# Performance work log

Measured on AMD Instinct MI355X. Metric: run time of the kernel, lower is better.

## Reference

```python
import jax, jax.numpy as jnp
import numpy as np

EPS = 1e-5
NUM_HEADS = 8

def _bn(x, w, b, m, v):
    # inference-mode BatchNorm2d over channel dim of (B,C,H,W)
    inv = w / jnp.sqrt(v + EPS)
    return x * inv[None, :, None, None] + (b - m * inv)[None, :, None, None]

def _conv1x1(x, W, b):
    # 1x1 conv == per-pixel matmul: W is (out_ch, in_ch)
    return jnp.einsum('bchw,ec->behw', x, W) + b[None, :, None, None]

def _forward(x, bn1_w, bn1_b, bn1_m, bn1_v, Wq, bq, Wk, bk, Wv, bv, gamma, temperature,
             conv_w, conv_b, cbn_w, cbn_b, cbn_m, cbn_v, rs_w, rs_b, rbn_w, rbn_b, rbn_m, rbn_v):
    B, C, Wd, Hd = x.shape
    S = Wd * Hd
    E = Wq.shape[0]
    hd = E // NUM_HEADS
    xa = jax.nn.relu(_bn(x, bn1_w, bn1_b, bn1_m, bn1_v))
    def proj(Wm, bm):
        return _conv1x1(xa, Wm, bm).reshape(B, NUM_HEADS, hd, S).transpose(0, 1, 3, 2)  # (B,h,S,d)
    q = proj(Wq, bq)
    k = proj(Wk, bk)
    v = proj(Wv, bv)
    scores = jnp.einsum('bhsd,bhtd->bhst', q, k) / temperature  # (B,h,S,S)
    scores = scores - jnp.max(scores, axis=-1, keepdims=True)   # redundant amax-subtract as in source
    attn = jax.nn.softmax(scores, axis=-1)
    out = jnp.einsum('bhst,bhtd->bhsd', attn, v)
    out = out.transpose(0, 1, 3, 2).reshape(B, E, Wd, Hd)
    conv_path = jax.nn.relu(_bn(_conv1x1(x, conv_w, conv_b), cbn_w, cbn_b, cbn_m, cbn_v))
    fused = gamma[0] * out + conv_path
    return jax.nn.gelu(_bn(_conv1x1(fused, rs_w, rs_b), rbn_w, rbn_b, rbn_m, rbn_v), approximate=False)

def setup_inputs() -> dict:
    key = jax.random.key(0)
    ks = jax.random.split(key, 18)
    C, E = 256, 512
    n = lambda k, s, sc=0.02: jax.random.normal(k, s, jnp.float32) * sc
    return {
        'x': jax.random.normal(ks[0], (1, C, 64, 64), jnp.float32),
        'bn1_w': 1.0 + n(ks[1], (C,), 0.1), 'bn1_b': n(ks[2], (C,), 0.1),
        'bn1_m': n(ks[3], (C,), 0.05), 'bn1_v': 0.5 + jax.random.uniform(ks[4], (C,), jnp.float32),
        'Wq': n(ks[5], (E, C)), 'bq': jnp.zeros((E,), jnp.float32),
        'Wk': n(ks[6], (E, C)), 'bk': jnp.zeros((E,), jnp.float32),
        'Wv': n(ks[7], (E, C)), 'bv': jnp.zeros((E,), jnp.float32),
        'gamma': jnp.full((1,), 0.5, jnp.float32),
        'temperature': jnp.asarray(0.85, jnp.float32),
        'conv_w': n(ks[8], (E, C)), 'conv_b': jnp.zeros((E,), jnp.float32),
        'cbn_w': 1.0 + n(ks[9], (E,), 0.1), 'cbn_b': n(ks[10], (E,), 0.1),
        'cbn_m': n(ks[11], (E,), 0.05), 'cbn_v': 0.5 + jax.random.uniform(ks[12], (E,), jnp.float32),
        'rs_w': n(ks[13], (C, E)), 'rs_b': jnp.zeros((C,), jnp.float32),
        'rbn_w': 1.0 + n(ks[14], (C,), 0.1), 'rbn_b': n(ks[15], (C,), 0.1),
        'rbn_m': n(ks[16], (C,), 0.05), 'rbn_v': 0.5 + jax.random.uniform(ks[17], (C,), jnp.float32),
    }

def reference(x, bn1_w, bn1_b, bn1_m, bn1_v, Wq, bq, Wk, bk, Wv, bv, gamma, temperature,
              conv_w, conv_b, cbn_w, cbn_b, cbn_m, cbn_v, rs_w, rs_b, rbn_w, rbn_b, rbn_m, rbn_v):
    return _forward(x, bn1_w, bn1_b, bn1_m, bn1_v, Wq, bq, Wk, bk, Wv, bv, gamma, temperature,
                    conv_w, conv_b, cbn_w, cbn_b, cbn_m, cbn_v, rs_w, rs_b, rbn_w, rbn_b, rbn_m, rbn_v)
```

## Files before the change

### kernel.cpp

```cpp
#include <hip/hip_runtime.h>

#define S_DIM 4096
#define C_IN  256
#define E_DIM 512
#define HD    64
#define EPSV  1e-5f

typedef __attribute__((ext_vector_type(8))) short s8v;
typedef __attribute__((ext_vector_type(4))) short s4v;
typedef __attribute__((ext_vector_type(4))) float f4v;
typedef __attribute__((ext_vector_type(16))) float f16v;

__device__ __forceinline__ float bf2f(unsigned short h){
  union{unsigned u; float f;} v; v.u = ((unsigned)h)<<16; return v.f;
}
__device__ __forceinline__ unsigned short f2bf(float f){
  union{float f; unsigned u;} v; v.f = f;
  unsigned r = v.u + 0x7fffu + ((v.u>>16)&1u);
  return (unsigned short)(r>>16);
}
__device__ __forceinline__ unsigned cvtpk_bf16(float lo, float hi_){
  unsigned r;
  asm("v_cvt_pk_bf16_f32 %0, %1, %2" : "=v"(r) : "v"(lo), "v"(hi_));
  return r;
}
__device__ __forceinline__ s8v lds_rd8(const unsigned short* b, int row, int ck){
  return *(const s8v*)&b[(row<<6) + (((ck)^(row&7))<<3)];
}
__device__ __forceinline__ s4v lds_rd4(const unsigned short* b, int row, int eoff){
  int ck = eoff>>3, sub = eoff&7;
  return *(const s4v*)&b[(row<<6) + ((ck^(row&7))<<3) + sub];
}
__device__ __forceinline__ void lds_wr8(unsigned short* b, int row, int ck, s8v v){
  *(s8v*)&b[(row<<6) + (((ck)^(row&7))<<3)] = v;
}

__global__ __launch_bounds__(256) void k_wcvt(const float* __restrict__ w0,
    const float* __restrict__ w1, const float* __restrict__ w2,
    const float* __restrict__ w3, const float* __restrict__ w4,
    unsigned short* __restrict__ dst){
  int i = blockIdx.x*256 + threadIdx.x;
  int z = blockIdx.y;
  const float* s = (z==0)?w0:(z==1)?w1:(z==2)?w2:(z==3)?w3:w4;
  dst[z*(E_DIM*C_IN) + i] = f2bf(s[i]);
}

__global__ __launch_bounds__(256) void k_prep(const float* __restrict__ x,
    const float* __restrict__ bw, const float* __restrict__ bb,
    const float* __restrict__ bm, const float* __restrict__ bvar,
    unsigned short* __restrict__ XaT, unsigned short* __restrict__ XrT){
  __shared__ float tile[32][33];
  int tid = threadIdx.x;
  int tx = tid & 31, ty = tid >> 5;
  int s0 = blockIdx.x*32, c0 = blockIdx.y*32;
  #pragma unroll
  for(int p=0;p<4;p++){
    int c = c0 + ty + p*8;
    tile[ty+p*8][tx] = x[c*S_DIM + s0 + tx];
  }
  __syncthreads();
  int cc = c0 + tx;
  float inv  = bw[cc] * rsqrtf(bvar[cc] + EPSV);
  float beta = bb[cc] - bm[cc]*inv;
  #pragma unroll
  for(int p=0;p<4;p++){
    int s = s0 + ty + p*8;
    float v = tile[tx][ty+p*8];
    float a = v*inv + beta; a = a>0.f?a:0.f;
    XaT[s*C_IN + cc] = f2bf(a);
    XrT[s*C_IN + cc] = f2bf(v);
  }
}

__global__ __launch_bounds__(256) void k_proj(
    const unsigned short* __restrict__ XaT, const unsigned short* __restrict__ XrT,
    const unsigned short* __restrict__ Wb,
    const float* __restrict__ bq, const float* __restrict__ bk,
    const float* __restrict__ bvb, const float* __restrict__ bc,
    const float* __restrict__ cw, const float* __restrict__ cbb,
    const float* __restrict__ cm, const float* __restrict__ cvv,
    unsigned short* __restrict__ QT, unsigned short* __restrict__ KT,
    unsigned short* __restrict__ Vx, unsigned short* __restrict__ CT){
  int z = blockIdx.z;
  const unsigned short* Xin = (z==3) ? XrT : XaT;
  const unsigned short* W   = Wb + z*(E_DIM*C_IN);
  const float* bias = (z==0)?bq:(z==1)?bk:(z==2)?bvb:bc;

  __shared__ unsigned short Als[128*64];
  __shared__ unsigned short Bls[64*64];
  int tid = threadIdx.x;
  int w = tid>>6, l = tid&63, g = l>>4, c16 = l&15;
  int wr = w>>1, wc = w&1;
  int s0 = blockIdx.x*128, e0 = blockIdx.y*64;

  f4v acc[4][2];
  #pragma unroll
  for(int m=0;m<4;m++)
    #pragma unroll
    for(int n=0;n<2;n++) acc[m][n] = (f4v){0.f,0.f,0.f,0.f};

  for(int kk=0;kk<4;kk++){
    __syncthreads();
    #pragma unroll
    for(int p=0;p<4;p++){
      int ck = p*256 + tid, row = ck>>3, ch = ck&7;
      s8v v = *(const s8v*)&Xin[(s0+row)*C_IN + kk*64 + ch*8];
      lds_wr8(Als, row, ch, v);
    }
    #pragma unroll
    for(int p=0;p<2;p++){
      int ck = p*256 + tid, row = ck>>3, ch = ck&7;
      s8v v = *(const s8v*)&W[(e0+row)*C_IN + kk*64 + ch*8];
      lds_wr8(Bls, row, ch, v);
    }
    __syncthreads();
    #pragma unroll
    for(int kb=0;kb<2;kb++){
      s8v bfr[2];
      #pragma unroll
      for(int n=0;n<2;n++) bfr[n] = lds_rd8(Bls, wc*32 + n*16 + c16, g + kb*4);
      #pragma unroll
      for(int m=0;m<4;m++){
        s8v af = lds_rd8(Als, wr*64 + m*16 + c16, g + kb*4);
        #pragma unroll
        for(int n=0;n<2;n++)
          acc[m][n] = __builtin_amdgcn_mfma_f32_16x16x32_bf16(af, bfr[n], acc[m][n], 0,0,0);
      }
    }
  }
  #pragma unroll
  for(int n=0;n<2;n++){
    int e = e0 + wc*32 + n*16 + c16;
    float bsv = bias[e];
    float cinv = 0.f, cbeta = 0.f;
    if(z==3){ cinv = cw[e]*rsqrtf(cvv[e]+EPSV); cbeta = cbb[e] - cm[e]*cinv; }
    #pragma unroll
    for(int m=0;m<4;m++){
      int sb = s0 + wr*64 + m*16 + g*4;
      if(z==2){
        s4v pk;
        #pragma unroll
        for(int i=0;i<4;i++) pk[i] = (short)f2bf(acc[m][n][i] + bsv);
        *(s4v*)&Vx[e*S_DIM + sb] = pk;
      } else {
        unsigned short* dst = (z==0)?QT:(z==1)?KT:CT;
        #pragma unroll
        for(int i=0;i<4;i++){
          float vv = acc[m][n][i] + bsv;
          if(z==3){ vv = vv*cinv + cbeta; vv = vv>0.f?vv:0.f; }
          dst[(sb+i)*E_DIM + e] = f2bf(vv);
        }
      }
    }
  }
}

__global__ __launch_bounds__(256) void k_attn(
    const unsigned short* __restrict__ QT, const unsigned short* __restrict__ KT,
    const unsigned short* __restrict__ Vx, const unsigned short* __restrict__ CT,
    const float* __restrict__ gamma, const float* __restrict__ temp,
    unsigned short* __restrict__ fusedT){
  __shared__ unsigned short SM[4*4096];
  int tid = threadIdx.x;
  int w = tid>>6, l = tid&63, l31 = l&31, hi = l>>5;
  int qh = w&1, kh = w>>1;
  int h = blockIdx.y;
  int qb = blockIdx.x*64;
  int q = qb + qh*32 + l31;
  float scl = 1.0f / temp[0];

  const unsigned short* Kb = SM + kh*4096;
  const unsigned short* Vb = SM + 8192 + kh*4096;

  s8v qf[4];
  #pragma unroll
  for(int ks=0;ks<4;ks++){
    s8v r = *(const s8v*)&QT[q*E_DIM + h*HD + ks*16 + hi*8];
    #pragma unroll
    for(int j=0;j<8;j++) qf[ks][j] = (short)f2bf(bf2f((unsigned short)r[j])*scl);
  }

  f16v oacc0, oacc1;
  #pragma unroll
  for(int r=0;r<16;r++){ oacc0[r]=0.f; oacc1[r]=0.f; }
  float lrun = 0.f;

  for(int t=0;t<32;t++){
    __syncthreads();
    #pragma unroll
    for(int p=0;p<8;p++){
      int flat = p*256 + tid;
      int tile = flat>>9, cid = flat&511, row = cid>>3, ch = cid&7;
      int khp = tile&1, isV = tile>>1;
      int sK = ((khp<<5) + t)<<6;
      s8v v;
      if(!isV) v = *(const s8v*)&KT[(sK+row)*E_DIM + h*HD + ch*8];
      else     v = *(const s8v*)&Vx[(h*HD+row)*S_DIM + sK + ch*8];
      lds_wr8(SM + tile*4096, row, ch, v);
    }
    __syncthreads();

    #pragma unroll
    for(int sub=0;sub<2;sub++){
      int krow = sub*32 + l31;
      f16v d;
      #pragma unroll
      for(int r=0;r<16;r++) d[r]=0.f;
      #pragma unroll
      for(int ks=0;ks<4;ks++){
        s8v kf = lds_rd8(Kb, krow, ks*2 + hi);
        d = __builtin_amdgcn_mfma_f32_32x32x16_bf16(kf, qf[ks], d, 0,0,0);
      }
      float e[16];
      float ls = 0.f;
      #pragma unroll
      for(int r=0;r<16;r++){ e[r] = __expf(d[r]); ls += e[r]; }
      lrun += ls;
      union{ s8v v; unsigned u[4]; } pa0, pa1;
      #pragma unroll
      for(int j=0;j<4;j++){
        pa0.u[j] = cvtpk_bf16(e[2*j],   e[2*j+1]);
        pa1.u[j] = cvtpk_bf16(e[8+2*j], e[8+2*j+1]);
      }
      #pragma unroll
      for(int dt=0;dt<2;dt++){
        int vrow = dt*32 + l31;
        union{ s8v v; s4v h2[2]; } vf;
        f16v& oa = dt ? oacc1 : oacc0;
        vf.h2[0] = lds_rd4(Vb, vrow, sub*32 + hi*4);
        vf.h2[1] = lds_rd4(Vb, vrow, sub*32 + hi*4 + 8);
        oa = __builtin_amdgcn_mfma_f32_32x32x16_bf16(pa0.v, vf.v, oa, 0,0,0);
        vf.h2[0] = lds_rd4(Vb, vrow, sub*32 + 16 + hi*4);
        vf.h2[1] = lds_rd4(Vb, vrow, sub*32 + 16 + hi*4 + 8);
        oa = __builtin_amdgcn_mfma_f32_32x32x16_bf16(pa1.v, vf.v, oa, 0,0,0);
      }
    }
  }

  lrun += __shfl_xor(lrun, 32);

  __syncthreads();
  float* mb = (float*)SM;
  float* l_lds = mb + 128*33;
  if(kh==1){
    float* dst = mb + (qh*64 + l)*33;
    #pragma unroll
    for(int r=0;r<16;r++){ dst[r] = oacc0[r]; dst[16+r] = oacc1[r]; }
    dst[32] = lrun;
  }
  __syncthreads();
  float ltot = 0.f;
  if(kh==0){
    const float* src = mb + (qh*64 + l)*33;
    #pragma unroll
    for(int r=0;r<16;r++){ oacc0[r] += src[r]; oacc1[r] += src[16+r]; }
    ltot = lrun + src[32];
  }
  if(kh==0 && hi==0) l_lds[qh*32 + l31] = ltot;
  __syncthreads();
  if(kh==0){
    float ga = gamma[0];
    #pragma unroll
    for(int dt=0;dt<2;dt++){
      const f16v& oa = dt ? oacc1 : oacc0;
      int e = h*HD + dt*32 + l31;
      #pragma unroll
      for(int g4=0;g4<4;g4++){
        float4 lv = *(float4*)&l_lds[qh*32 + g4*8 + hi*4];
        float la[4] = {lv.x, lv.y, lv.z, lv.w};
        #pragma unroll
        for(int j=0;j<4;j++){
          int r = g4*4 + j;
          int qrow = qb + qh*32 + j + g4*8 + hi*4;
          float o = oa[r]/la[j]*ga + bf2f(CT[qrow*E_DIM + e]);
          fusedT[qrow*E_DIM + e] = f2bf(o);
        }
      }
    }
  }
}

__global__ __launch_bounds__(256) void k_final(
    const unsigned short* __restrict__ Wrs,
    const unsigned short* __restrict__ fusedT,
    const float* __restrict__ rsb,
    const float* __restrict__ rw, const float* __restrict__ rbb,
    const float* __restrict__ rm, const float* __restrict__ rv,
    float* __restrict__ out){
  __shared__ unsigned short Als[64*64];
  __shared__ unsigned short Bls[128*64];
  int tid = threadIdx.x;
  int w = tid>>6, l = tid&63, g = l>>4, c16 = l&15;
  int wr = w>>1, wc = w&1;
  int sB0 = blockIdx.x*128, c0 = blockIdx.y*64;
  f4v acc[2][4];
  #pragma unroll
  for(int m=0;m<2;m++)
    #pragma unroll
    for(int n=0;n<4;n++) acc[m][n]=(f4v){0.f,0.f,0.f,0.f};
  for(int kk=0;kk<8;kk++){
    __syncthreads();
    #pragma unroll
    for(int p=0;p<2;p++){
      int ck = p*256+tid, row=ck>>3, ch=ck&7;
      s8v v = *(const s8v*)&Wrs[(c0+row)*E_DIM + kk*64 + ch*8];
      lds_wr8(Als, row, ch, v);
    }
    #pragma unroll
    for(int p=0;p<4;p++){
      int ck = p*256+tid, row=ck>>3, ch=ck&7;
      s8v v = *(const s8v*)&fusedT[(sB0+row)*E_DIM + kk*64 + ch*8];
      lds_wr8(Bls, row, ch, v);
    }
    __syncthreads();
    #pragma unroll
    for(int kb=0;kb<2;kb++){
      s8v af[2]; s8v bfr[4];
      #pragma unroll
      for(int m=0;m<2;m++) af[m] = lds_rd8(Als, wr*32 + m*16 + c16, g + kb*4);
      #pragma unroll
      for(int n=0;n<4;n++) bfr[n] = lds_rd8(Bls, wc*64 + n*16 + c16, g + kb*4);
      #pragma unroll
      for(int m=0;m<2;m++)
        #pragma unroll
        for(int n=0;n<4;n++)
          acc[m][n] = __builtin_amdgcn_mfma_f32_16x16x32_bf16(af[m], bfr[n], acc[m][n],0,0,0);
    }
  }
  #pragma unroll
  for(int m=0;m<2;m++){
    #pragma unroll
    for(int i=0;i<4;i++){
      int c = c0 + wr*32 + m*16 + g*4 + i;
      float bias = rsb[c];
      float rinv = rw[c]*rsqrtf(rv[c]+EPSV);
      float rbeta = rbb[c] - rm[c]*rinv;
      #pragma unroll
      for(int n=0;n<4;n++){
        int s = sB0 + wc*64 + n*16 + c16;
        float vv = acc[m][n][i] + bias;
        vv = vv*rinv + rbeta;
        out[c*S_DIM + s] = 0.5f*vv*(1.0f + erff(vv*0.70710678118f));
      }
    }
  }
}

extern "C" void kernel_launch(void* const* d_in, const int* in_sizes, int n_in,
                              void* d_out, int out_size, void* d_ws, size_t ws_size,
                              hipStream_t stream){
  const float* x     = (const float*)d_in[0];
  const float* bn1w  = (const float*)d_in[1];
  const float* bn1b  = (const float*)d_in[2];
  const float* bn1m  = (const float*)d_in[3];
  const float* bn1v  = (const float*)d_in[4];
  const float* Wq    = (const float*)d_in[5];
  const float* bq    = (const float*)d_in[6];
  const float* Wk    = (const float*)d_in[7];
  const float* bk    = (const float*)d_in[8];
  const float* Wv    = (const float*)d_in[9];
  const float* bv    = (const float*)d_in[10];
  const float* gamma = (const float*)d_in[11];
  const float* temp  = (const float*)d_in[12];
  const float* convw = (const float*)d_in[13];
  const float* convb = (const float*)d_in[14];
  const float* cbnw  = (const float*)d_in[15];
  const float* cbnb  = (const float*)d_in[16];
  const float* cbnm  = (const float*)d_in[17];
  const float* cbnv  = (const float*)d_in[18];
  const float* rsw   = (const float*)d_in[19];
  const float* rsbp  = (const float*)d_in[20];
  const float* rbnw  = (const float*)d_in[21];
  const float* rbnb  = (const float*)d_in[22];
  const float* rbnm  = (const float*)d_in[23];
  const float* rbnv  = (const float*)d_in[24];
  float* out = (float*)d_out;

  unsigned short* ws  = (unsigned short*)d_ws;
  unsigned short* XaT = ws;
  unsigned short* XrT = XaT + S_DIM*C_IN;
  unsigned short* Wb  = XrT + S_DIM*C_IN;
  unsigned short* Wrs = Wb + 4*E_DIM*C_IN;
  unsigned short* QT  = Wrs + C_IN*E_DIM;
  unsigned short* KT  = QT + S_DIM*E_DIM;
  unsigned short* Vx  = KT + S_DIM*E_DIM;
  unsigned short* CT  = Vx + S_DIM*E_DIM;
  unsigned short* fusedT = CT + S_DIM*E_DIM;

  k_wcvt<<<dim3(512,5),256,0,stream>>>(Wq, Wk, Wv, convw, rsw, Wb);
  k_prep<<<dim3(128,8),256,0,stream>>>(x, bn1w, bn1b, bn1m, bn1v, XaT, XrT);
  k_proj<<<dim3(32,8,4),256,0,stream>>>(XaT, XrT, Wb, bq, bk, bv, convb,
                                        cbnw, cbnb, cbnm, cbnv, QT, KT, Vx, CT);
  k_attn<<<dim3(64,8),256,0,stream>>>(QT, KT, Vx, CT, gamma, temp, fusedT);
  k_final<<<dim3(32,4),256,0,stream>>>(Wrs, fusedT, rsbp, rbnw, rbnb, rbnm, rbnv, out);
}
```

Baseline: 94.64 us.

## Double query tile per attention block, prefetch K/V to registers, retile final GEMM

```diff
diff --git a/kernel.cpp b/kernel.cpp
--- a/kernel.cpp
+++ b/kernel.cpp
@@ -27,12 +27,14 @@
 __device__ __forceinline__ s8v lds_rd8(const unsigned short* b, int row, int ck){
   return *(const s8v*)&b[(row<<6) + (((ck)^(row&7))<<3)];
 }
-__device__ __forceinline__ s4v lds_rd4(const unsigned short* b, int row, int eoff){
-  int ck = eoff>>3, sub = eoff&7;
-  return *(const s4v*)&b[(row<<6) + ((ck^(row&7))<<3) + sub];
-}
 __device__ __forceinline__ void lds_wr8(unsigned short* b, int row, int ck, s8v v){
   *(s8v*)&b[(row<<6) + (((ck)^(row&7))<<3)] = v;
+}
+__device__ __forceinline__ s4v lds_rd4q(const unsigned short* b, int row, int q4){
+  return *(const s4v*)&b[(row<<6) + (((q4)^(row&15))<<2)];
+}
+__device__ __forceinline__ void lds_wr4q(unsigned short* b, int row, int q4, s4v v){
+  *(s4v*)&b[(row<<6) + (((q4)^(row&15))<<2)] = v;
 }
 
 __global__ __launch_bounds__(256) void k_wcvt(const float* __restrict__ w0,
@@ -155,125 +157,175 @@
   }
 }
 
-__global__ __launch_bounds__(256) void k_attn(
+__global__ __launch_bounds__(256,1) void k_attn(
     const unsigned short* __restrict__ QT, const unsigned short* __restrict__ KT,
     const unsigned short* __restrict__ Vx, const unsigned short* __restrict__ CT,
     const float* __restrict__ gamma, const float* __restrict__ temp,
     unsigned short* __restrict__ fusedT){
-  __shared__ unsigned short SM[4*4096];
+  __shared__ unsigned short SM[16384];
   int tid = threadIdx.x;
   int w = tid>>6, l = tid&63, l31 = l&31, hi = l>>5;
   int qh = w&1, kh = w>>1;
-  int h = blockIdx.y;
-  int qb = blockIdx.x*64;
-  int q = qb + qh*32 + l31;
+  int fb = blockIdx.y*32 + blockIdx.x;
+  int h = fb&7;
+  int qb = (fb>>3)*128;
   float scl = 1.0f / temp[0];
 
   const unsigned short* Kb = SM + kh*4096;
   const unsigned short* Vb = SM + 8192 + kh*4096;
 
-  s8v qf[4];
-  #pragma unroll
-  for(int ks=0;ks<4;ks++){
-    s8v r = *(const s8v*)&QT[q*E_DIM + h*HD + ks*16 + hi*8];
-    #pragma unroll
-    for(int j=0;j<8;j++) qf[ks][j] = (short)f2bf(bf2f((unsigned short)r[j])*scl);
-  }
-
-  f16v oacc0, oacc1;
-  #pragma unroll
-  for(int r=0;r<16;r++){ oacc0[r]=0.f; oacc1[r]=0.f; }
-  float lrun = 0.f;
+  s8v qf[2][4];
+  #pragma unroll
+  for(int qg=0;qg<2;qg++){
+    int q = qb + qh*64 + qg*32 + l31;
+    #pragma unroll
+    for(int ks=0;ks<4;ks++){
+      s8v r = *(const s8v*)&QT[q*E_DIM + h*HD + ks*16 + hi*8];
+      #pragma unroll
+      for(int j=0;j<8;j++) qf[qg][ks][j] = (short)f2bf(bf2f((unsigned short)r[j])*scl);
+    }
+  }
+
+  f16v oacc[2][2];
+  #pragma unroll
+  for(int qg=0;qg<2;qg++)
+    #pragma unroll
+    for(int dt=0;dt<2;dt++)
+      #pragma unroll
+      for(int r=0;r<16;r++) oacc[qg][dt][r]=0.f;
+  float lrun[2] = {0.f, 0.f};
+
+  int krow = tid>>2, kch2 = (tid&3)*2;
+  int vrow = (tid&511)>>3, vch = tid&7;
+
+  s8v kreg[4], vreg[4];
+  #pragma unroll
+  for(int p=0;p<2;p++){
+    #pragma unroll
+    for(int kp=0;kp<1;kp++){}
+  }
+  #pragma unroll
+  for(int p=0;p<4;p++){
+    int flat = p*256 + tid, kp = flat>>9, cid = flat&511, row = cid>>3, ch = cid&7;
+    kreg[p] = *(const s8v*)&KT[((kp*32 + 0)*64 + row)*E_DIM + h*HD + ch*8];
+  }
+  #pragma unroll
+  for(int p=0;p<4;p++){
+    int flat = p*256 + tid, kp = flat>>9, cid = flat&511, row = cid>>3, ch = cid&7;
+    vreg[p] = *(const s8v*)&Vx[(h*HD + row)*S_DIM + (kp*32 + 0)*64 + ch*8];
+  }
 
   for(int t=0;t<32;t++){
     __syncthreads();
     #pragma unroll
-    for(int p=0;p<8;p++){
-      int flat = p*256 + tid;
-      int tile = flat>>9, cid = flat&511, row = cid>>3, ch = cid&7;
-      int khp = tile&1, isV = tile>>1;
-      int sK = ((khp<<5) + t)<<6;
-      s8v v;
-      if(!isV) v = *(const s8v*)&KT[(sK+row)*E_DIM + h*HD + ch*8];
-      else     v = *(const s8v*)&Vx[(h*HD+row)*S_DIM + sK + ch*8];
-      lds_wr8(SM + tile*4096, row, ch, v);
-    }
-    __syncthreads();
+    for(int p=0;p<4;p++){
+      int flat = p*256 + tid, kp = flat>>9, cid = flat&511, row = cid>>3, ch = cid&7;
+      lds_wr8((unsigned short*)SM + kp*4096, row, ch, kreg[p]);
+    }
+    #pragma unroll
+    for(int p=0;p<4;p++){
+      int flat = p*256 + tid, kp = flat>>9, cid = flat&511, row = cid>>3, ch = cid&7;
+      union{ s8v v; s4v h2[2]; } u; u.v = vreg[p];
+      unsigned short* Vt = (unsigned short*)SM + 8192 + kp*4096;
+      lds_wr4q(Vt, row, ch*2,   u.h2[0]);
+      lds_wr4q(Vt, row, ch*2+1, u.h2[1]);
+    }
+    __syncthreads();
+    if(t < 31){
+      #pragma unroll
+      for(int p=0;p<4;p++){
+        int flat = p*256 + tid, kp = flat>>9, cid = flat&511, row = cid>>3, ch = cid&7;
+        kreg[p] = *(const s8v*)&KT[((kp*32 + t+1)*64 + row)*E_DIM + h*HD + ch*8];
+      }
+      #pragma unroll
+      for(int p=0;p<4;p++){
+        int flat = p*256 + tid, kp = flat>>9, cid = flat&511, row = cid>>3, ch = cid&7;
+        vreg[p] = *(const s8v*)&Vx[(h*HD + row)*S_DIM + (kp*32 + t+1)*64 + ch*8];
+      }
+    }
 
     #pragma unroll
     for(int sub=0;sub<2;sub++){
-      int krow = sub*32 + l31;
-      f16v d;
-      #pragma unroll
-      for(int r=0;r<16;r++) d[r]=0.f;
-      #pragma unroll
-      for(int ks=0;ks<4;ks++){
-        s8v kf = lds_rd8(Kb, krow, ks*2 + hi);
-        d = __builtin_amdgcn_mfma_f32_32x32x16_bf16(kf, qf[ks], d, 0,0,0);
-      }
-      float e[16];
-      float ls = 0.f;
-      #pragma unroll
-      for(int r=0;r<16;r++){ e[r] = __expf(d[r]); ls += e[r]; }
-      lrun += ls;
-      union{ s8v v; unsigned u[4]; } pa0, pa1;
-      #pragma unroll
-      for(int j=0;j<4;j++){
-        pa0.u[j] = cvtpk_bf16(e[2*j],   e[2*j+1]);
-        pa1.u[j] = cvtpk_bf16(e[8+2*j], e[8+2*j+1]);
+      int kr = sub*32 + l31;
+      s8v kf[4];
+      #pragma unroll
+      for(int ks=0;ks<4;ks++) kf[ks] = lds_rd8(Kb, kr, ks*2 + hi);
+
+      union{ s8v v; unsigned u[4]; } pa[2][2];
+      #pragma unroll
+      for(int qg=0;qg<2;qg++){
+        f16v d;
+        #pragma unroll
+        for(int r=0;r<16;r++) d[r]=0.f;
+        #pragma unroll
+        for(int ks=0;ks<4;ks++)
+          d = __builtin_amdgcn_mfma_f32_32x32x16_bf16(kf[ks], qf[qg][ks], d, 0,0,0);
+        float e[16], ls = 0.f;
+        #pragma unroll
+        for(int r=0;r<16;r++){ e[r] = __expf(d[r]); ls += e[r]; }
+        lrun[qg] += ls;
+        #pragma unroll
+        for(int j=0;j<4;j++){
+          pa[qg][0].u[j] = cvtpk_bf16(e[2*j],   e[2*j+1]);
+          pa[qg][1].u[j] = cvtpk_bf16(e[8+2*j], e[8+2*j+1]);
+        }
       }
       #pragma unroll
       for(int dt=0;dt<2;dt++){
-        int vrow = dt*32 + l31;
+        int vr = dt*32 + l31;
         union{ s8v v; s4v h2[2]; } vf;
-        f16v& oa = dt ? oacc1 : oacc0;
-        vf.h2[0] = lds_rd4(Vb, vrow, sub*32 + hi*4);
-        vf.h2[1] = lds_rd4(Vb, vrow, sub*32 + hi*4 + 8);
-        oa = __builtin_amdgcn_mfma_f32_32x32x16_bf16(pa0.v, vf.v, oa, 0,0,0);
-        vf.h2[0] = lds_rd4(Vb, vrow, sub*32 + 16 + hi*4);
-        vf.h2[1] = lds_rd4(Vb, vrow, sub*32 + 16 + hi*4 + 8);
-        oa = __builtin_amdgcn_mfma_f32_32x32x16_bf16(pa1.v, vf.v, oa, 0,0,0);
-      }
-    }
-  }
-
-  lrun += __shfl_xor(lrun, 32);
-
-  __syncthreads();
+        vf.h2[0] = lds_rd4q(Vb, vr, sub*8 + hi);
+        vf.h2[1] = lds_rd4q(Vb, vr, sub*8 + 2 + hi);
+        oacc[0][dt] = __builtin_amdgcn_mfma_f32_32x32x16_bf16(pa[0][0].v, vf.v, oacc[0][dt], 0,0,0);
+        oacc[1][dt] = __builtin_amdgcn_mfma_f32_32x32x16_bf16(pa[1][0].v, vf.v, oacc[1][dt], 0,0,0);
+        vf.h2[0] = lds_rd4q(Vb, vr, sub*8 + 4 + hi);
+        vf.h2[1] = lds_rd4q(Vb, vr, sub*8 + 6 + hi);
+        oacc[0][dt] = __builtin_amdgcn_mfma_f32_32x32x16_bf16(pa[0][1].v, vf.v, oacc[0][dt], 0,0,0);
+        oacc[1][dt] = __builtin_amdgcn_mfma_f32_32x32x16_bf16(pa[1][1].v, vf.v, oacc[1][dt], 0,0,0);
+      }
+    }
+  }
+
+  #pragma unroll
+  for(int qg=0;qg<2;qg++) lrun[qg] += __shfl_xor(lrun[qg], 32);
+
   float* mb = (float*)SM;
-  float* l_lds = mb + 128*33;
-  if(kh==1){
-    float* dst = mb + (qh*64 + l)*33;
-    #pragma unroll
-    for(int r=0;r<16;r++){ dst[r] = oacc0[r]; dst[16+r] = oacc1[r]; }
-    dst[32] = lrun;
-  }
-  __syncthreads();
-  float ltot = 0.f;
-  if(kh==0){
-    const float* src = mb + (qh*64 + l)*33;
-    #pragma unroll
-    for(int r=0;r<16;r++){ oacc0[r] += src[r]; oacc1[r] += src[16+r]; }
-    ltot = lrun + src[32];
-  }
-  if(kh==0 && hi==0) l_lds[qh*32 + l31] = ltot;
-  __syncthreads();
-  if(kh==0){
-    float ga = gamma[0];
-    #pragma unroll
-    for(int dt=0;dt<2;dt++){
-      const f16v& oa = dt ? oacc1 : oacc0;
-      int e = h*HD + dt*32 + l31;
-      #pragma unroll
-      for(int g4=0;g4<4;g4++){
-        float4 lv = *(float4*)&l_lds[qh*32 + g4*8 + hi*4];
-        float la[4] = {lv.x, lv.y, lv.z, lv.w};
-        #pragma unroll
-        for(int j=0;j<4;j++){
-          int r = g4*4 + j;
-          int qrow = qb + qh*32 + j + g4*8 + hi*4;
-          float o = oa[r]/la[j]*ga + bf2f(CT[qrow*E_DIM + e]);
-          fusedT[qrow*E_DIM + e] = f2bf(o);
+  float* l_buf = mb + 4224;
+  float ga = gamma[0];
+  #pragma unroll
+  for(int qg=0;qg<2;qg++){
+    __syncthreads();
+    if(kh==1){
+      float* dst = mb + (qh*64 + l)*33;
+      #pragma unroll
+      for(int r=0;r<16;r++){ dst[r] = oacc[qg][0][r]; dst[16+r] = oacc[qg][1][r]; }
+      dst[32] = lrun[qg];
+    }
+    __syncthreads();
+    float ltot = 0.f;
+    if(kh==0){
+      const float* src = mb + (qh*64 + l)*33;
+      #pragma unroll
+      for(int r=0;r<16;r++){ oacc[qg][0][r] += src[r]; oacc[qg][1][r] += src[16+r]; }
+      ltot = lrun[qg] + src[32];
+      if(hi==0) l_buf[qh*32 + l31] = ltot;
+    }
+    __syncthreads();
+    if(kh==0){
+      #pragma unroll
+      for(int dt=0;dt<2;dt++){
+        int e = h*HD + dt*32 + l31;
+        #pragma unroll
+        for(int g4=0;g4<4;g4++){
+          float4 lv = *(float4*)&l_buf[qh*32 + g4*8 + hi*4];
+          float la[4] = {lv.x, lv.y, lv.z, lv.w};
+          #pragma unroll
+          for(int j=0;j<4;j++){
+            int r = g4*4 + j;
+            int qrow = qb + qh*64 + qg*32 + j + g4*8 + hi*4;
+            float o = oacc[qg][dt][r]/la[j]*ga + bf2f(CT[qrow*E_DIM + e]);
+            fusedT[qrow*E_DIM + e] = f2bf(o);
+          }
         }
       }
     }
@@ -288,16 +340,16 @@
     const float* __restrict__ rm, const float* __restrict__ rv,
     float* __restrict__ out){
   __shared__ unsigned short Als[64*64];
-  __shared__ unsigned short Bls[128*64];
+  __shared__ unsigned short Bls[64*64];
   int tid = threadIdx.x;
   int w = tid>>6, l = tid&63, g = l>>4, c16 = l&15;
-  int wr = w>>1, wc = w&1;
-  int sB0 = blockIdx.x*128, c0 = blockIdx.y*64;
-  f4v acc[2][4];
+  int wr2 = w>>1, wc2 = w&1;
+  int sB0 = blockIdx.x*64, c0 = blockIdx.y*64;
+  f4v acc[2][2];
   #pragma unroll
   for(int m=0;m<2;m++)
     #pragma unroll
-    for(int n=0;n<4;n++) acc[m][n]=(f4v){0.f,0.f,0.f,0.f};
+    for(int n=0;n<2;n++) acc[m][n]=(f4v){0.f,0.f,0.f,0.f};
   for(int kk=0;kk<8;kk++){
     __syncthreads();
     #pragma unroll
@@ -307,7 +359,7 @@
       lds_wr8(Als, row, ch, v);
     }
     #pragma unroll
-    for(int p=0;p<4;p++){
+    for(int p=0;p<2;p++){
       int ck = p*256+tid, row=ck>>3, ch=ck&7;
       s8v v = *(const s8v*)&fusedT[(sB0+row)*E_DIM + kk*64 + ch*8];
       lds_wr8(Bls, row, ch, v);
@@ -315,15 +367,15 @@
     __syncthreads();
     #pragma unroll
     for(int kb=0;kb<2;kb++){
-      s8v af[2]; s8v bfr[4];
-      #pragma unroll
-      for(int m=0;m<2;m++) af[m] = lds_rd8(Als, wr*32 + m*16 + c16, g + kb*4);
-      #pragma unroll
-      for(int n=0;n<4;n++) bfr[n] = lds_rd8(Bls, wc*64 + n*16 + c16, g + kb*4);
+      s8v af[2]; s8v bfr[2];
+      #pragma unroll
+      for(int m=0;m<2;m++) af[m] = lds_rd8(Als, wr2*32 + m*16 + c16, g + kb*4);
+      #pragma unroll
+      for(int n=0;n<2;n++) bfr[n] = lds_rd8(Bls, wc2*32 + n*16 + c16, g + kb*4);
       #pragma unroll
       for(int m=0;m<2;m++)
         #pragma unroll
-        for(int n=0;n<4;n++)
+        for(int n=0;n<2;n++)
           acc[m][n] = __builtin_amdgcn_mfma_f32_16x16x32_bf16(af[m], bfr[n], acc[m][n],0,0,0);
     }
   }
@@ -331,13 +383,13 @@
   for(int m=0;m<2;m++){
     #pragma unroll
     for(int i=0;i<4;i++){
-      int c = c0 + wr*32 + m*16 + g*4 + i;
+      int c = c0 + wr2*32 + m*16 + g*4 + i;
       float bias = rsb[c];
       float rinv = rw[c]*rsqrtf(rv[c]+EPSV);
       float rbeta = rbb[c] - rm[c]*rinv;
       #pragma unroll
-      for(int n=0;n<4;n++){
-        int s = sB0 + wc*64 + n*16 + c16;
+      for(int n=0;n<2;n++){
+        int s = sB0 + wc2*32 + n*16 + c16;
         float vv = acc[m][n][i] + bias;
         vv = vv*rinv + rbeta;
         out[c*S_DIM + s] = 0.5f*vv*(1.0f + erff(vv*0.70710678118f));
@@ -391,6 +443,6 @@
   k_prep<<<dim3(128,8),256,0,stream>>>(x, bn1w, bn1b, bn1m, bn1v, XaT, XrT);
   k_proj<<<dim3(32,8,4),256,0,stream>>>(XaT, XrT, Wb, bq, bk, bv, convb,
                                         cbnw, cbnb, cbnm, cbnv, QT, KT, Vx, CT);
-  k_attn<<<dim3(64,8),256,0,stream>>>(QT, KT, Vx, CT, gamma, temp, fusedT);
-  k_final<<<dim3(32,4),256,0,stream>>>(Wrs, fusedT, rsbp, rbnw, rbnb, rbnm, rbnv, out);
-}
+  k_attn<<<dim3(32,8),256,0,stream>>>(QT, KT, Vx, CT, gamma, temp, fusedT);
+  k_final<<<dim3(64,4),256,0,stream>>>(Wrs, fusedT, rsbp, rbnw, rbnb, rbnm, rbnv, out);
+}
```

Measured after the change: 94.26 us. No clear change (-0.4%).
